# Kernel optimization log

Measured on AMD Instinct MI355X. Metric: run time of the kernel, lower is better.

## Reference

```python
import jax, jax.numpy as jnp
import numpy as np

B, S, E, FEAT, ATT, NCLS, VOCAB = 32, 512, 512, 256, 10, 8, 32000
# NOTE: original code requires S == E (attentive_content [S,S] assigned into a [S,E] buffer)


def setup_inputs() -> dict:
    key = jax.random.key(0)
    ks = jax.random.split(key, 8)
    x = jax.random.randint(ks[0], (B, S), 0, VOCAB)
    emb = jax.random.normal(ks[1], (VOCAB, E), dtype=jnp.float32) * 0.02
    A = jax.random.uniform(ks[2], (E, ATT), dtype=jnp.float32, minval=-0.1, maxval=0.1)
    Wh = jax.random.normal(ks[3], (FEAT, E, 3), dtype=jnp.float32) * 0.02   # h_conv, k=3, no bias
    Wc = jax.random.normal(ks[4], (FEAT, E), dtype=jnp.float32) * 0.02      # c_conv, k=1, no bias
    tanh_bias = jnp.zeros((FEAT,), dtype=jnp.float32)
    Wfc = jax.random.normal(ks[5], (NCLS, FEAT), dtype=jnp.float32) * 0.02
    bfc = jnp.zeros((NCLS,), dtype=jnp.float32)
    return {"x": x, "emb": emb, "A": A, "Wh": Wh, "Wc": Wc,
            "tanh_bias": tanh_bias, "Wfc": Wfc, "bfc": bfc}


def reference(x, emb, A, Wh, Wc, tanh_bias, Wfc, bfc):
    ex = emb[x]                                    # [B,S,E] embedding lookup
    # batched version of the per-sample loop: mm -> softmax -> mm
    scores = jnp.einsum('bse,ea->bsa', ex, A)      # [B,S,ATT]
    attn = jax.nn.softmax(scores, axis=-1)         # softmax over attention dim (2D default)
    att = jnp.einsum('bsa,bta->bst', attn, scores)  # [B,S,S]  (S == E)
    # h branch: conv1d(k=3, valid) over time, then global max-pool
    h = jax.lax.conv_general_dilated(ex.transpose(0, 2, 1), Wh, (1,), 'VALID',
                                     dimension_numbers=('NCH', 'OIH', 'NCH'))  # [B,F,S-2]
    h = jnp.max(h, axis=-1)                        # [B,F]
    # c branch: k=1 conv over att (permuted), i.e. channel mix, then global max-pool
    c = jnp.max(jnp.einsum('blc,fc->bfl', att, Wc), axis=-1)  # [B,F]
    out = jnp.tanh(h + c + tanh_bias)
    return out @ Wfc.T + bfc                       # [B,num_class]
```

## Files before the change

kernel.cpp:

```cpp
#include <hip/hip_runtime.h>
#include <math.h>

#define B 32
#define S 512
#define E 512
#define FEAT 256
#define ATT 10
#define NCLS 8

using short8 = __attribute__((ext_vector_type(8))) short;
using f32x4  = __attribute__((ext_vector_type(4))) float;

__device__ __forceinline__ unsigned short f2bf(float f) {
    unsigned int u = __float_as_uint(f);
    return (unsigned short)((u + 0x7fffu + ((u >> 16) & 1u)) >> 16);
}

__device__ __forceinline__ void gl16(const void* g, void* l) {
    __builtin_amdgcn_global_load_lds(
        (const __attribute__((address_space(1))) unsigned int*)g,
        (__attribute__((address_space(3))) unsigned int*)l, 16, 0, 0);
}

__global__ __launch_bounds__(256) void k_front(
        const int* __restrict__ x, const float* __restrict__ emb,
        const float* __restrict__ A, const float* __restrict__ Wh,
        unsigned short* __restrict__ ex16, unsigned short* __restrict__ Whk16,
        float* __restrict__ sc12, float* __restrict__ at12) {
    const int blk = blockIdx.x;
    const int tid = threadIdx.x;
    if (blk < 2048) {
        const int wave = tid >> 6, lane = tid & 63;
        f32x4 av4[20];
        const f32x4* ap4 = (const f32x4*)(A + (size_t)lane * 80);
#pragma unroll
        for (int q = 0; q < 20; ++q) av4[q] = ap4[q];
#pragma unroll
        for (int rep = 0; rep < 2; ++rep) {
            const int bs = blk * 8 + wave * 2 + rep;
            const int row = x[bs];
            const f32x4* src = (const f32x4*)(emb + (size_t)row * E);
            const f32x4 v0 = src[lane * 2], v1 = src[lane * 2 + 1];
            float v[8] = {v0[0], v0[1], v0[2], v0[3], v1[0], v1[1], v1[2], v1[3]};

            short8 sv;
#pragma unroll
            for (int j = 0; j < 8; ++j) sv[j] = (short)f2bf(v[j]);
            *(short8*)(ex16 + (size_t)bs * E + lane * 8) = sv;

            float acc[ATT] = {};
#pragma unroll
            for (int j = 0; j < 8; ++j)
#pragma unroll
                for (int a = 0; a < ATT; ++a) {
                    const int idx = j * ATT + a;
                    acc[a] = fmaf(v[j], av4[idx >> 2][idx & 3], acc[a]);
                }
#pragma unroll
            for (int a = 0; a < ATT; ++a)
#pragma unroll
                for (int off = 1; off < 64; off <<= 1) acc[a] += __shfl_xor(acc[a], off);

            if (lane == 0) {
                float m = -1e30f;
#pragma unroll
                for (int a = 0; a < ATT; ++a) m = fmaxf(m, acc[a]);
                float ev[ATT], sum = 0.f;
#pragma unroll
                for (int a = 0; a < ATT; ++a) { ev[a] = expf(acc[a] - m); sum += ev[a]; }
                const float inv = 1.f / sum;
                float* sp = sc12 + (size_t)bs * 12;
                float* tp = at12 + (size_t)bs * 12;
                *(f32x4*)(sp)     = (f32x4){acc[0], acc[1], acc[2], acc[3]};
                *(f32x4*)(sp + 4) = (f32x4){acc[4], acc[5], acc[6], acc[7]};
                *(f32x4*)(sp + 8) = (f32x4){acc[8], acc[9], 0.f, 0.f};
                *(f32x4*)(tp)     = (f32x4){ev[0] * inv, ev[1] * inv, ev[2] * inv, ev[3] * inv};
                *(f32x4*)(tp + 4) = (f32x4){ev[4] * inv, ev[5] * inv, ev[6] * inv, ev[7] * inv};
                *(f32x4*)(tp + 8) = (f32x4){ev[8] * inv, ev[9] * inv, 0.f, 0.f};
            }
        }
    } else if (blk < 2048 + FEAT) {
        const int f = blk - 2048;
        const float* src = Wh + (size_t)f * (E * 3);
        unsigned short* dst = Whk16 + (size_t)f * (E * 3);
#pragma unroll
        for (int i = 0; i < 6; ++i) {
            const int kk = tid + i * 256;
            dst[kk] = f2bf(src[(kk & 511) * 3 + (kk >> 9)]);
        }
        if (f == 0) {
            for (int i = tid; i < 2 * E; i += 256) ex16[(size_t)B * S * E + i] = 0;
        }
    }
}

__global__ __launch_bounds__(256) void k_conv(const unsigned short* __restrict__ Whk,
                                              const unsigned short* __restrict__ ex16,
                                              float* __restrict__ Cpart) {
    __shared__ unsigned short lds[2][32768];
    const int b = blockIdx.x;
    const int fbase = blockIdx.y * 128;
    const int lbase = blockIdx.z * 128;
    const int tid = threadIdx.x;
    const int wave = tid >> 6, lane = tid & 63;
    const int wm = wave >> 1, wn = wave & 1;
    const int lane15 = lane & 15, g4 = lane >> 4;
    const int r4 = lane >> 4;
    const int slot = lane & 15;
    const unsigned short* exb = ex16 + (size_t)b * S * E;

    f32x4 acc[4][4];
#pragma unroll
    for (int mf = 0; mf < 4; ++mf)
#pragma unroll
        for (int nf = 0; nf < 4; ++nf) acc[mf][nf] = (f32x4){0.f, 0.f, 0.f, 0.f};

    auto stage = [&](int t, unsigned short* buf) {
        const int kk0 = t << 7;
        const int kpc = t >> 2;
        const int e0  = (t & 3) << 7;
        unsigned short* la = buf;
        unsigned short* lb = buf + 16384;
#pragma unroll
        for (int ii = 0; ii < 8; ++ii) {
            const int r = wave * 32 + ii * 4 + r4;
            gl16(Whk + (size_t)(fbase + r) * 1536 + kk0 + ((slot ^ (r & 7)) << 3),
                 la + (wave * 8 + ii) * 512);
        }
#pragma unroll
        for (int ii = 0; ii < 8; ++ii) {
            const int r = wave * 32 + ii * 4 + r4;
            gl16(exb + (size_t)(lbase + r + kpc) * E + e0 + ((slot ^ (r & 7)) << 3),
                 lb + (wave * 8 + ii) * 512);
        }
    };

    auto compute = [&](const unsigned short* buf) {
        const char* la = (const char*)buf;
        const char* lb = (const char*)(buf + 16384);
#pragma unroll
        for (int kh = 0; kh < 4; ++kh) {
            short8 av[4], bv[4];
#pragma unroll
            for (int mf = 0; mf < 4; ++mf) {
                const int row = wm * 64 + mf * 16 + lane15;
                av[mf] = *(const short8*)(la + row * 256 +
                                          ((((kh << 2) | g4) ^ (row & 7)) << 4));
            }
#pragma unroll
            for (int nf = 0; nf < 4; ++nf) {
                const int row = wn * 64 + nf * 16 + lane15;
                bv[nf] = *(const short8*)(lb + row * 256 +
                                          ((((kh << 2) | g4) ^ (row & 7)) << 4));
            }
#pragma unroll
            for (int mf = 0; mf < 4; ++mf)
#pragma unroll
                for (int nf = 0; nf < 4; ++nf)
                    acc[mf][nf] = __builtin_amdgcn_mfma_f32_16x16x32_bf16(
                        av[mf], bv[nf], acc[mf][nf], 0, 0, 0);
        }
    };

    stage(0, lds[0]);
    asm volatile("s_waitcnt vmcnt(0)" ::: "memory");
    __builtin_amdgcn_s_barrier();

    for (int t = 0; t < 12; ++t) {
        if (t + 1 < 12) stage(t + 1, lds[(t + 1) & 1]);
        compute(lds[t & 1]);
        if (t + 1 < 12) {
            asm volatile("s_waitcnt vmcnt(0)" ::: "memory");
            __builtin_amdgcn_s_barrier();
        }
    }

#pragma unroll
    for (int mf = 0; mf < 4; ++mf) {
#pragma unroll
        for (int j = 0; j < 4; ++j) {
            float m = -1e30f;
#pragma unroll
            for (int nf = 0; nf < 4; ++nf) {
                const int l = lbase + wn * 64 + nf * 16 + lane15;
                if (l < S - 2) m = fmaxf(m, acc[mf][nf][j]);
            }
#pragma unroll
            for (int off = 1; off < 16; off <<= 1) m = fmaxf(m, __shfl_xor(m, off));
            if (lane15 == 0) {
                const int f = fbase + wm * 64 + mf * 16 + g4 * 4 + j;
                Cpart[(((size_t)b * FEAT + f) << 3) + blockIdx.z * 2 + wn] = m;
            }
        }
    }
}

__global__ __launch_bounds__(256) void k_chc(
        const float* __restrict__ sc12, const float* __restrict__ at12,
        const float* __restrict__ Wc, const float* __restrict__ Cpart,
        const float* __restrict__ tb, float* __restrict__ hc) {
    const int fg = blockIdx.x, b = blockIdx.y;
    const int wave = threadIdx.x >> 6, lane = threadIdx.x & 63;
    const int f0 = fg * 32 + wave * 8;

    f32x4 wc[8][2];
#pragma unroll
    for (int ff = 0; ff < 8; ++ff) {
        const float* wp = Wc + (size_t)(f0 + ff) * E + lane * 8;
        wc[ff][0] = *(const f32x4*)wp;
        wc[ff][1] = *(const f32x4*)(wp + 4);
    }

    f32x4 g[8][3];
#pragma unroll
    for (int ff = 0; ff < 8; ++ff)
#pragma unroll
        for (int q = 0; q < 3; ++q) g[ff][q] = (f32x4){0.f, 0.f, 0.f, 0.f};

    const f32x4* scp = (const f32x4*)(sc12 + (size_t)b * S * 12);
#pragma unroll
    for (int j = 0; j < 8; ++j) {
        const int t = lane * 8 + j;
        const f32x4 s0 = scp[t * 3], s1 = scp[t * 3 + 1], s2 = scp[t * 3 + 2];
#pragma unroll
        for (int ff = 0; ff < 8; ++ff) {
            const float w = wc[ff][j >> 2][j & 3];
            g[ff][0] += s0 * w; g[ff][1] += s1 * w; g[ff][2] += s2 * w;
        }
    }
#pragma unroll
    for (int ff = 0; ff < 8; ++ff)
#pragma unroll
        for (int q = 0; q < 3; ++q)
#pragma unroll
            for (int c = 0; c < 4; ++c)
#pragma unroll
                for (int off = 1; off < 64; off <<= 1)
                    g[ff][q][c] += __shfl_xor(g[ff][q][c], off);

    const f32x4* atp = (const f32x4*)(at12 + (size_t)b * S * 12);
    float mc[8];
#pragma unroll
    for (int ff = 0; ff < 8; ++ff) mc[ff] = -1e30f;
#pragma unroll
    for (int j = 0; j < 8; ++j) {
        const int t = lane * 8 + j;
        const f32x4 a0 = atp[t * 3], a1 = atp[t * 3 + 1], a2 = atp[t * 3 + 2];
#pragma unroll
        for (int ff = 0; ff < 8; ++ff) {
            const f32x4 p = a0 * g[ff][0] + a1 * g[ff][1] + a2 * g[ff][2];
            mc[ff] = fmaxf(mc[ff], p[0] + p[1] + p[2] + p[3]);
        }
    }
#pragma unroll
    for (int ff = 0; ff < 8; ++ff)
#pragma unroll
        for (int off = 1; off < 64; off <<= 1)
            mc[ff] = fmaxf(mc[ff], __shfl_xor(mc[ff], off));

    if (lane == 0) {
#pragma unroll
        for (int ff = 0; ff < 8; ++ff) {
            const int f = f0 + ff;
            const float* cp = Cpart + (((size_t)b * FEAT + f) << 3);
            float mh = cp[0];
#pragma unroll
            for (int q = 1; q < 8; ++q) mh = fmaxf(mh, cp[q]);
            hc[(size_t)b * FEAT + f] = tanhf(mh + mc[ff] + tb[f]);
        }
    }
}

__global__ void k_out(const float* __restrict__ hc, const float* __restrict__ Wfc,
                      const float* __restrict__ bfc, float* __restrict__ out) {
    const int b = blockIdx.x;
    const int tid = threadIdx.x;
    __shared__ float hv[FEAT];
    __shared__ float ps[256];
    hv[tid] = hc[(size_t)b * FEAT + tid];
    __syncthreads();
    const int n = tid & 7;
    const int c = tid >> 3;
    float p = 0.f;
#pragma unroll
    for (int q = 0; q < 8; ++q) p = fmaf(hv[c * 8 + q], Wfc[(size_t)n * FEAT + c * 8 + q], p);
    ps[tid] = p;
    __syncthreads();
    if (tid < 8) {
        float s = bfc[tid];
        for (int q = 0; q < 32; ++q) s += ps[tid + 8 * q];
        out[(size_t)b * NCLS + tid] = s;
    }
}

extern "C" void kernel_launch(void* const* d_in, const int* in_sizes, int n_in,
                              void* d_out, int out_size, void* d_ws, size_t ws_size,
                              hipStream_t stream) {
    const int* x      = (const int*)d_in[0];
    const float* emb  = (const float*)d_in[1];
    const float* A    = (const float*)d_in[2];
    const float* Wh   = (const float*)d_in[3];
    const float* Wc   = (const float*)d_in[4];
    const float* tb   = (const float*)d_in[5];
    const float* Wfc  = (const float*)d_in[6];
    const float* bfc  = (const float*)d_in[7];
    float* out = (float*)d_out;

    unsigned short* ex16  = (unsigned short*)d_ws;
    unsigned short* Whk16 = ex16 + (size_t)B * S * E + 2 * E;
    float* sc12 = (float*)(Whk16 + (size_t)FEAT * 3 * E);
    float* at12 = sc12 + (size_t)B * S * 12;
    float* Cpart = at12 + (size_t)B * S * 12;
    float* hc    = Cpart + (size_t)B * FEAT * 8;

    k_front<<<2048 + FEAT, 256, 0, stream>>>(x, emb, A, Wh, ex16, Whk16, sc12, at12);
    k_conv<<<dim3(B, 2, 4), 256, 0, stream>>>(Whk16, ex16, Cpart);
    k_chc<<<dim3(8, B), 256, 0, stream>>>(sc12, at12, Wc, Cpart, tb, hc);
    k_out<<<B, 256, 0, stream>>>(hc, Wfc, bfc, out);
}
```

Baseline: 66.65 us.

## Split conv K across two wave groups and fuse output FC into chc

The conv kernel moves to 512 threads, with two groups of four waves each handling half of the 1536-long reduction over 64-wide K steps. Their accumulators are summed through LDS before the max-pool. Separately, the final FC kernel is removed: chc computes partial logits per feature group and atomically adds them into the output, which the front kernel now initialises with the bias. This cuts one launch and doubles the waves per conv block, at the cost of an LDS reduction and atomics whose summation order is nondeterministic.

```diff
diff --git a/kernel.cpp b/kernel.cpp
--- a/kernel.cpp
+++ b/kernel.cpp
@@ -25,8 +25,10 @@
 __global__ __launch_bounds__(256) void k_front(
         const int* __restrict__ x, const float* __restrict__ emb,
         const float* __restrict__ A, const float* __restrict__ Wh,
-        unsigned short* __restrict__ ex16, unsigned short* __restrict__ Whk16,
-        float* __restrict__ sc12, float* __restrict__ at12) {
+        const float* __restrict__ bfc, unsigned short* __restrict__ ex16,
+        unsigned short* __restrict__ Whk16,
+        float* __restrict__ sc12, float* __restrict__ at12,
+        float* __restrict__ out) {
     const int blk = blockIdx.x;
     const int tid = threadIdx.x;
     if (blk < 2048) {
@@ -91,22 +93,26 @@
         if (f == 0) {
             for (int i = tid; i < 2 * E; i += 256) ex16[(size_t)B * S * E + i] = 0;
         }
-    }
-}
-
-__global__ __launch_bounds__(256) void k_conv(const unsigned short* __restrict__ Whk,
+    } else {
+        if (tid < B * NCLS) out[tid] = bfc[tid & 7];
+    }
+}
+
+__global__ __launch_bounds__(512) void k_conv(const unsigned short* __restrict__ Whk,
                                               const unsigned short* __restrict__ ex16,
                                               float* __restrict__ Cpart) {
-    __shared__ unsigned short lds[2][32768];
+    __shared__ __align__(16) unsigned short lds[2][32768];
     const int b = blockIdx.x;
     const int fbase = blockIdx.y * 128;
     const int lbase = blockIdx.z * 128;
     const int tid = threadIdx.x;
     const int wave = tid >> 6, lane = tid & 63;
-    const int wm = wave >> 1, wn = wave & 1;
+    const int g = wave >> 2;
+    const int sub = wave & 3;
+    const int wm = sub >> 1, wn = sub & 1;
     const int lane15 = lane & 15, g4 = lane >> 4;
-    const int r4 = lane >> 4;
-    const int slot = lane & 15;
+    const int tg = sub * 64 + lane;
+    const int rr = tg >> 3, slot = tg & 7;
     const unsigned short* exb = ex16 + (size_t)b * S * E;
 
     f32x4 acc[4][4];
@@ -116,41 +122,37 @@
         for (int nf = 0; nf < 4; ++nf) acc[mf][nf] = (f32x4){0.f, 0.f, 0.f, 0.f};
 
     auto stage = [&](int t, unsigned short* buf) {
-        const int kk0 = t << 7;
-        const int kpc = t >> 2;
-        const int e0  = (t & 3) << 7;
-        unsigned short* la = buf;
-        unsigned short* lb = buf + 16384;
-#pragma unroll
-        for (int ii = 0; ii < 8; ++ii) {
-            const int r = wave * 32 + ii * 4 + r4;
-            gl16(Whk + (size_t)(fbase + r) * 1536 + kk0 + ((slot ^ (r & 7)) << 3),
-                 la + (wave * 8 + ii) * 512);
-        }
-#pragma unroll
-        for (int ii = 0; ii < 8; ++ii) {
-            const int r = wave * 32 + ii * 4 + r4;
-            gl16(exb + (size_t)(lbase + r + kpc) * E + e0 + ((slot ^ (r & 7)) << 3),
-                 lb + (wave * 8 + ii) * 512);
+        const int kkg = g * 768 + (t << 6);
+        const int tap = kkg >> 9;
+        const int e0  = kkg & 511;
+        unsigned short* la = buf + g * 16384;
+        unsigned short* lb = la + 8192;
+#pragma unroll
+        for (int i = 0; i < 4; ++i) {
+            const int r = i * 32 + rr;
+            gl16(Whk + (size_t)(fbase + r) * 1536 + kkg + ((slot ^ (r & 7)) << 3),
+                 la + i * 2048 + sub * 512);
+            gl16(exb + (size_t)(lbase + r + tap) * E + e0 + ((slot ^ (r & 7)) << 3),
+                 lb + i * 2048 + sub * 512);
         }
     };
 
     auto compute = [&](const unsigned short* buf) {
-        const char* la = (const char*)buf;
-        const char* lb = (const char*)(buf + 16384);
-#pragma unroll
-        for (int kh = 0; kh < 4; ++kh) {
+        const char* la = (const char*)(buf + g * 16384);
+        const char* lb = la + 16384;
+#pragma unroll
+        for (int kh = 0; kh < 2; ++kh) {
             short8 av[4], bv[4];
 #pragma unroll
             for (int mf = 0; mf < 4; ++mf) {
                 const int row = wm * 64 + mf * 16 + lane15;
-                av[mf] = *(const short8*)(la + row * 256 +
+                av[mf] = *(const short8*)(la + row * 128 +
                                           ((((kh << 2) | g4) ^ (row & 7)) << 4));
             }
 #pragma unroll
             for (int nf = 0; nf < 4; ++nf) {
                 const int row = wn * 64 + nf * 16 + lane15;
-                bv[nf] = *(const short8*)(lb + row * 256 +
+                bv[nf] = *(const short8*)(lb + row * 128 +
                                           ((((kh << 2) | g4) ^ (row & 7)) << 4));
             }
 #pragma unroll
@@ -175,21 +177,39 @@
         }
     }
 
-#pragma unroll
-    for (int mf = 0; mf < 4; ++mf) {
-#pragma unroll
-        for (int j = 0; j < 4; ++j) {
-            float m = -1e30f;
-#pragma unroll
-            for (int nf = 0; nf < 4; ++nf) {
-                const int l = lbase + wn * 64 + nf * 16 + lane15;
-                if (l < S - 2) m = fmaxf(m, acc[mf][nf][j]);
-            }
-#pragma unroll
-            for (int off = 1; off < 16; off <<= 1) m = fmaxf(m, __shfl_xor(m, off));
-            if (lane15 == 0) {
-                const int f = fbase + wm * 64 + mf * 16 + g4 * 4 + j;
-                Cpart[(((size_t)b * FEAT + f) << 3) + blockIdx.z * 2 + wn] = m;
+    __syncthreads();
+    f32x4* lf = (f32x4*)&lds[0][0];
+    if (g == 1) {
+#pragma unroll
+        for (int mf = 0; mf < 4; ++mf)
+#pragma unroll
+            for (int nf = 0; nf < 4; ++nf)
+                lf[(mf * 4 + nf) * 256 + sub * 64 + lane] = acc[mf][nf];
+    }
+    __syncthreads();
+    if (g == 0) {
+#pragma unroll
+        for (int mf = 0; mf < 4; ++mf)
+#pragma unroll
+            for (int nf = 0; nf < 4; ++nf)
+                acc[mf][nf] += lf[(mf * 4 + nf) * 256 + sub * 64 + lane];
+
+#pragma unroll
+        for (int mf = 0; mf < 4; ++mf) {
+#pragma unroll
+            for (int j = 0; j < 4; ++j) {
+                float m = -1e30f;
+#pragma unroll
+                for (int nf = 0; nf < 4; ++nf) {
+                    const int l = lbase + wn * 64 + nf * 16 + lane15;
+                    if (l < S - 2) m = fmaxf(m, acc[mf][nf][j]);
+                }
+#pragma unroll
+                for (int off = 1; off < 16; off <<= 1) m = fmaxf(m, __shfl_xor(m, off));
+                if (lane15 == 0) {
+                    const int f = fbase + wm * 64 + mf * 16 + g4 * 4 + j;
+                    Cpart[(((size_t)b * FEAT + f) << 3) + blockIdx.z * 2 + wn] = m;
+                }
             }
         }
     }
@@ -198,10 +218,14 @@
 __global__ __launch_bounds__(256) void k_chc(
         const float* __restrict__ sc12, const float* __restrict__ at12,
         const float* __restrict__ Wc, const float* __restrict__ Cpart,
-        const float* __restrict__ tb, float* __restrict__ hc) {
+        const float* __restrict__ tb, const float* __restrict__ Wfc,
+        float* __restrict__ out) {
     const int fg = blockIdx.x, b = blockIdx.y;
-    const int wave = threadIdx.x >> 6, lane = threadIdx.x & 63;
+    const int tid = threadIdx.x;
+    const int wave = tid >> 6, lane = tid & 63;
     const int f0 = fg * 32 + wave * 8;
+    __shared__ float shc[32];
+    __shared__ float ps[256];
 
     f32x4 wc[8][2];
 #pragma unroll
@@ -266,30 +290,19 @@
             float mh = cp[0];
 #pragma unroll
             for (int q = 1; q < 8; ++q) mh = fmaxf(mh, cp[q]);
-            hc[(size_t)b * FEAT + f] = tanhf(mh + mc[ff] + tb[f]);
-        }
-    }
-}
-
-__global__ void k_out(const float* __restrict__ hc, const float* __restrict__ Wfc,
-                      const float* __restrict__ bfc, float* __restrict__ out) {
-    const int b = blockIdx.x;
-    const int tid = threadIdx.x;
-    __shared__ float hv[FEAT];
-    __shared__ float ps[256];
-    hv[tid] = hc[(size_t)b * FEAT + tid];
+            shc[wave * 8 + ff] = tanhf(mh + mc[ff] + tb[f]);
+        }
+    }
     __syncthreads();
-    const int n = tid & 7;
-    const int c = tid >> 3;
-    float p = 0.f;
-#pragma unroll
-    for (int q = 0; q < 8; ++q) p = fmaf(hv[c * 8 + q], Wfc[(size_t)n * FEAT + c * 8 + q], p);
-    ps[tid] = p;
+
+    const int n = tid & 7, fl = tid >> 3;
+    ps[tid] = shc[fl] * Wfc[(size_t)n * FEAT + fg * 32 + fl];
     __syncthreads();
     if (tid < 8) {
-        float s = bfc[tid];
+        float s = 0.f;
+#pragma unroll
         for (int q = 0; q < 32; ++q) s += ps[tid + 8 * q];
-        out[(size_t)b * NCLS + tid] = s;
+        atomicAdd(&out[b * NCLS + tid], s);
     }
 }
 
@@ -311,10 +324,9 @@
     float* sc12 = (float*)(Whk16 + (size_t)FEAT * 3 * E);
     float* at12 = sc12 + (size_t)B * S * 12;
     float* Cpart = at12 + (size_t)B * S * 12;
-    float* hc    = Cpart + (size_t)B * FEAT * 8;
-
-    k_front<<<2048 + FEAT, 256, 0, stream>>>(x, emb, A, Wh, ex16, Whk16, sc12, at12);
-    k_conv<<<dim3(B, 2, 4), 256, 0, stream>>>(Whk16, ex16, Cpart);
-    k_chc<<<dim3(8, B), 256, 0, stream>>>(sc12, at12, Wc, Cpart, tb, hc);
-    k_out<<<B, 256, 0, stream>>>(hc, Wfc, bfc, out);
-}
+
+    k_front<<<2048 + FEAT + 1, 256, 0, stream>>>(x, emb, A, Wh, bfc,
+                                                 ex16, Whk16, sc12, at12, out);
+    k_conv<<<dim3(B, 2, 4), 512, 0, stream>>>(Whk16, ex16, Cpart);
+    k_chc<<<dim3(8, B), 256, 0, stream>>>(sc12, at12, Wc, Cpart, tb, Wfc, out);
+}
```

Measured after the change: 62.74 us. 5.9% less time.
